# Kernel tuning notes

Measured on AMD Instinct MI355X. Metric: run time of the kernel, lower is better.

Reference implementation:

```python
import jax, jax.numpy as jnp
import numpy as np

B, T, C, H = 4, 2048, 1024, 16
HS = C // H  # head_size = 64


def setup_inputs() -> dict:
    key = jax.random.key(0)
    ks = jax.random.split(key, 6)
    s = C ** -0.5  # Linear default init scale (approx, kaiming-uniform-ish)
    x = jax.random.normal(ks[0], (B, T, C), dtype=jnp.float32)
    Wq = jax.random.normal(ks[1], (H, C, HS), dtype=jnp.float32) * s
    Wk = jax.random.normal(ks[2], (H, C, HS), dtype=jnp.float32) * s
    Wv = jax.random.normal(ks[3], (H, C, HS), dtype=jnp.float32) * s
    Wproj = jax.random.normal(ks[4], (C, C), dtype=jnp.float32) * s
    bproj = jax.random.normal(ks[5], (C,), dtype=jnp.float32) * s
    return {"x": x, "Wq": Wq, "Wk": Wk, "Wv": Wv, "Wproj": Wproj, "bproj": bproj}


def reference(x, Wq, Wk, Wv, Wproj, bproj):
    # Batched multi-head attention equivalent to looping over per-head modules.
    # q,k,v: (B, H, T, HS)
    q = jnp.einsum('btc,hcd->bhtd', x, Wq)
    k = jnp.einsum('btc,hcd->bhtd', x, Wk)
    v = jnp.einsum('btc,hcd->bhtd', x, Wv)
    scale = HS ** -0.5
    scores = jnp.einsum('bhqd,bhkd->bhqk', q, k) * scale  # (B,H,T,T)
    causal = jnp.tril(jnp.ones((T, T), dtype=bool))
    scores = jnp.where(causal, scores, -jnp.inf)
    wei = jax.nn.softmax(scores, axis=-1)
    out_heads = jnp.einsum('bhqk,bhkd->bhqd', wei, v)  # (B,H,T,HS)
    # concat heads along last dim -> (B,T,H*HS) = (B,T,C)
    combo = out_heads.transpose(0, 2, 1, 3).reshape(B, T, C)
    out = jnp.einsum('btc,cd->btd', combo, Wproj.T.T @ jnp.eye(C, dtype=combo.dtype)) if False else combo @ Wproj.T + bproj
    # dropout p=0.0 (eval) -> identity
    return out
```

## Files before the change

### kernel.cpp

```cpp
#include <hip/hip_runtime.h>
#include <stdint.h>

#define B_  4
#define T_  2048
#define C_  1024
#define H_  16
#define HS_ 64
#define M_  (B_*T_)
#define K_  C_

typedef unsigned short u16;
typedef float v4f __attribute__((ext_vector_type(4)));
typedef short v8s __attribute__((ext_vector_type(8)));
typedef u16   v4u __attribute__((ext_vector_type(4)));
typedef unsigned int u32;
typedef u32 v2u32 __attribute__((ext_vector_type(2)));

__device__ __forceinline__ u16 f2bf(float f){
  unsigned u = __float_as_uint(f);
  u += 0x7fffu + ((u >> 16) & 1u);
  return (u16)(u >> 16);
}

__device__ __forceinline__ u32 cvt_pk_bf16(float a, float b){
  u32 r;
  asm("v_cvt_pk_bf16_f32 %0, %1, %2" : "=v"(r) : "v"(a), "v"(b));
  return r;
}

__device__ __forceinline__ void async16(const void* g, void* l){
  __builtin_amdgcn_global_load_lds(
      (const __attribute__((address_space(1))) unsigned int*)g,
      (__attribute__((address_space(3))) unsigned int*)l,
      16, 0, 0);
}


__global__ void conv_blocked(const float* __restrict__ src, u16* __restrict__ dst){
  int gid = blockIdx.x * 256 + threadIdx.x;
  int r  = gid >> 7;
  int kg = gid & 127;
  const float* s = src + ((size_t)r << 10) + (kg << 3);
  v4f a = *(const v4f*)s;
  v4f b = *(const v4f*)(s + 4);
  union { v8s v; u16 e[8]; } o;
  o.e[0]=f2bf(a[0]); o.e[1]=f2bf(a[1]); o.e[2]=f2bf(a[2]); o.e[3]=f2bf(a[3]);
  o.e[4]=f2bf(b[0]); o.e[5]=f2bf(b[1]); o.e[6]=f2bf(b[2]); o.e[7]=f2bf(b[3]);
  *(v8s*)(dst + (((size_t)(r >> 4) * 128 + kg) * 128 + ((r & 15) << 3))) = o.v;
}

__global__ void transpose_w(const float* __restrict__ Wq, const float* __restrict__ Wk,
                            const float* __restrict__ Wv, u16* __restrict__ wallT){
  int idx = blockIdx.x * 256 + threadIdx.x;
  int n = idx >> 10, c = idx & 1023;
  int tensor = n >> 10;
  int h = (n >> 6) & 15;
  int d = n & 63;
  const float* W = (tensor == 0) ? Wq : ((tensor == 1) ? Wk : Wv);
  wallT[((size_t)(n >> 4) * 128 + (c >> 3)) * 128 + ((n & 15) << 3) + (c & 7)]
      = f2bf(W[((size_t)(h * C_ + c)) * HS_ + d]);
}

#define QSCALE 0.1803368801111204f

template<int MODE>
__global__ __launch_bounds__(256)
void gemm_bt(const u16* __restrict__ A, const u16* __restrict__ Bt,
             const float* __restrict__ bias,
             u16* __restrict__ o0, u16* __restrict__ o1, u16* __restrict__ o2,
             float* __restrict__ o0f)
{
  __shared__ __align__(16) u16 sA[2][128 * 32];
  __shared__ __align__(16) u16 sB[2][128 * 32];
  const int tid  = threadIdx.x;
  const int lane = tid & 63;
  const int wave = tid >> 6;
  const int l15  = lane & 15, quad = lane >> 4;
  const int wm   = wave >> 1, wn = wave & 1;
  const int m0   = blockIdx.y * 128;
  const int n0   = blockIdx.x * 128;
  const int mg0  = blockIdx.y * 8;
  const int ng0  = blockIdx.x * 8;

  v4f acc[4][4] = {};

  const int s0 = tid, s1 = tid + 256;
  const int t0 = s0 >> 6, r0 = s0 & 15, g0 = (s0 >> 4) & 3;
  const int t1 = s1 >> 6, r1 = s1 & 15, g1 = (s1 >> 4) & 3;

  const char* aS0 = (const char*)A  + ((size_t)(mg0 + t0) * 16384 + g0 * 128 + r0 * 8) * 2;
  const char* aS1 = (const char*)A  + ((size_t)(mg0 + t1) * 16384 + g1 * 128 + r1 * 8) * 2;
  const char* bS0 = (const char*)Bt + ((size_t)(ng0 + t0) * 16384 + g0 * 128 + r0 * 8) * 2;
  const char* bS1 = (const char*)Bt + ((size_t)(ng0 + t1) * 16384 + g1 * 128 + r1 * 8) * 2;

  async16(aS0, (char*)sA[0] + s0 * 16);
  async16(aS1, (char*)sA[0] + s1 * 16);
  async16(bS0, (char*)sB[0] + s0 * 16);
  async16(bS1, (char*)sB[0] + s1 * 16);
  __syncthreads();

  int cur = 0;
  for (int kk = 0; kk < K_; kk += 32){
    const int nxt = cur ^ 1;
    if (kk + 32 < K_){
      const size_t off = (size_t)(kk + 32) * 32;
      async16(aS0 + off, (char*)sA[nxt] + s0 * 16);
      async16(aS1 + off, (char*)sA[nxt] + s1 * 16);
      async16(bS0 + off, (char*)sB[nxt] + s0 * 16);
      async16(bS1 + off, (char*)sB[nxt] + s1 * 16);
    }

    v8s af[4], bfr[4];
    const u16* pa = sA[cur] + (size_t)(wm * 4) * 512 + lane * 8;
    const u16* pb = sB[cur] + (size_t)(wn * 4) * 512 + lane * 8;
    #pragma unroll
    for (int mi = 0; mi < 4; mi++) af[mi]  = *(const v8s*)(pa + mi * 512);
    #pragma unroll
    for (int ni = 0; ni < 4; ni++) bfr[ni] = *(const v8s*)(pb + ni * 512);

    #pragma unroll
    for (int mi = 0; mi < 4; mi++)
      #pragma unroll
      for (int ni = 0; ni < 4; ni++)
        acc[mi][ni] = __builtin_amdgcn_mfma_f32_16x16x32_bf16(af[mi], bfr[ni], acc[mi][ni], 0, 0, 0);

    __syncthreads();
    cur = nxt;
  }

  if constexpr (MODE == 0){
    #pragma unroll
    for (int ni = 0; ni < 4; ni++){
      const int ng = n0 + wn * 64 + ni * 16 + l15;
      const int tensor = ng >> 10;
      const int hh = (ng >> 6) & 15;
      const int d  = ng & 63;
      #pragma unroll
      for (int mi = 0; mi < 4; mi++){
        const int mbase = m0 + wm * 64 + mi * 16 + quad * 4;
        const int bb = mbase >> 11;
        const int tt = mbase & 2047;
        if (tensor == 2){
          v4u pk;
          #pragma unroll
          for (int r = 0; r < 4; r++) pk[r] = f2bf(acc[mi][ni][r]);
          *(v4u*)(o2 + ((size_t)((bb * H_ + hh) * HS_ + d)) * T_ + tt) = pk;
        } else if (tensor == 0){
          #pragma unroll
          for (int r = 0; r < 4; r++)
            o0[((size_t)((bb * H_ + hh)) * T_ + tt + r) * HS_ + d] = f2bf(acc[mi][ni][r] * QSCALE);
        } else {
          #pragma unroll
          for (int r = 0; r < 4; r++)
            o1[((size_t)((bb * H_ + hh)) * T_ + tt + r) * HS_ + d] = f2bf(acc[mi][ni][r]);
        }
      }
    }
  } else {
    #pragma unroll
    for (int ni = 0; ni < 4; ni++){
      const int ng = n0 + wn * 64 + ni * 16 + l15;
      const float bv = bias[ng];
      #pragma unroll
      for (int mi = 0; mi < 4; mi++){
        const int mbase = m0 + wm * 64 + mi * 16 + quad * 4;
        #pragma unroll
        for (int r = 0; r < 4; r++)
          o0f[(size_t)(mbase + r) * C_ + ng] = acc[mi][ni][r] + bv;
      }
    }
  }
}

__global__ __launch_bounds__(512, 4)
void attn(const u16* __restrict__ Q, const u16* __restrict__ Kb_, const u16* __restrict__ Vt,
          u16* __restrict__ O)
{
  __shared__ __align__(16) u16 sK[64 * 64];
  __shared__ __align__(16) u16 sV[64 * 64];
  __shared__ __align__(16) u16 Plds[8][16][88];
  const int tid  = threadIdx.x;
  const int lane = tid & 63;
  const int wave = tid >> 6;
  const int l15  = lane & 15, quad = lane >> 4;
  const int pp   = blockIdx.y & 7;
  const int bh   = blockIdx.x * 8 + (blockIdx.y >> 3);

  const u16* Qb = Q   + (size_t)bh * T_ * HS_;
  const u16* Kb = Kb_ + (size_t)bh * T_ * HS_;
  const u16* Vb = Vt  + (size_t)bh * HS_ * T_;
  const int b = bh >> 4, h = bh & 15;

  const int g  = tid;
  const int tg = g >> 3;
  const int sw = ((g & 7) ^ (tg & 7)) << 4;
  const char* Kby = (const char*)Kb;
  const char* Vby = (const char*)Vb;
  const int koff = tg * 128 + sw;
  const int voff = tg * (T_ * 2) + sw;
  char* sKp = (char*)sK + g * 16;
  char* sVp = (char*)sV + g * 16;

  const int fsw0 = (quad ^ (l15 & 7)) * 8;
  const int fsw1 = ((quad + 4) ^ (l15 & 7)) * 8;

  #pragma unroll 1
  for (int ph = 0; ph < 2; ph++){
    const int qt = ph ? (15 - pp) : pp;
    const int q0 = qt * 128 + wave * 16;

    const v8s qf0 = *(const v8s*)(Qb + (size_t)(q0 + l15) * HS_ + quad * 8);
    const v8s qf1 = *(const v8s*)(Qb + (size_t)(q0 + l15) * HS_ + 32 + quad * 8);

    v4f Oa[4] = {};
    float lsum = 0.f;

    const int ktmax = 2 * qt + 1;
    for (int kt = 0; kt <= ktmax; kt++){
      const int k0 = kt * 64;
      async16(Kby + (size_t)k0 * 128 + koff, sKp);
      async16(Vby + (size_t)k0 * 2   + voff, sVp);
      __syncthreads();

      if (k0 <= q0 + 15){
        v4f sacc[4] = {};
        __builtin_amdgcn_s_setprio(1);
        #pragma unroll
        for (int nt = 0; nt < 4; nt++){
          const u16* kr = sK + (nt * 16 + l15) * 64;
          v8s kf0 = *(const v8s*)(kr + fsw0);
          v8s kf1 = *(const v8s*)(kr + fsw1);
          sacc[nt] = __builtin_amdgcn_mfma_f32_16x16x32_bf16(kf0, qf0, sacc[nt], 0, 0, 0);
          sacc[nt] = __builtin_amdgcn_mfma_f32_16x16x32_bf16(kf1, qf1, sacc[nt], 0, 0, 0);
        }
        __builtin_amdgcn_s_setprio(0);
        const bool diag = (k0 + 63 > q0);
        const int qrow_rel = (q0 - k0) + l15;

        #pragma unroll
        for (int nt = 0; nt < 4; nt++){
          float p0 = exp2f(sacc[nt][0]);
          float p1 = exp2f(sacc[nt][1]);
          float p2 = exp2f(sacc[nt][2]);
          float p3 = exp2f(sacc[nt][3]);
          if (diag){
            const int kbase = nt * 16 + quad * 4;
            if (kbase + 0 > qrow_rel) p0 = 0.f;
            if (kbase + 1 > qrow_rel) p1 = 0.f;
            if (kbase + 2 > qrow_rel) p2 = 0.f;
            if (kbase + 3 > qrow_rel) p3 = 0.f;
          }
          lsum += (p0 + p1) + (p2 + p3);
          v2u32 w;
          w[0] = cvt_pk_bf16(p0, p1);
          w[1] = cvt_pk_bf16(p2, p3);
          *(v2u32*)&Plds[wave][l15][nt * 16 + quad * 4] = w;
        }

        asm volatile("" ::: "memory");
        const v8s pf0 = *(const v8s*)&Plds[wave][l15][quad * 8];
        const v8s pf1 = *(const v8s*)&Plds[wave][l15][32 + quad * 8];
        __builtin_amdgcn_s_setprio(1);
        #pragma unroll
        for (int nt = 0; nt < 4; nt++){
          const u16* vr = sV + (nt * 16 + l15) * 64;
          v8s vf0 = *(const v8s*)(vr + fsw0);
          v8s vf1 = *(const v8s*)(vr + fsw1);
          Oa[nt] = __builtin_amdgcn_mfma_f32_16x16x32_bf16(pf0, vf0, Oa[nt], 0, 0, 0);
          Oa[nt] = __builtin_amdgcn_mfma_f32_16x16x32_bf16(pf1, vf1, Oa[nt], 0, 0, 0);
        }
        __builtin_amdgcn_s_setprio(0);
      }
      __syncthreads();
    }

    float rs = lsum;
    rs += __shfl_xor(rs, 16);
    rs += __shfl_xor(rs, 32);
    const int mg = b * 128 + qt * 8 + wave;
    #pragma unroll
    for (int reg = 0; reg < 4; reg++){
      const float rsq = __shfl(rs, quad * 4 + reg);
      const float inv = (rsq > 0.f) ? (1.f / rsq) : 0.f;
      const int mrow = quad * 4 + reg;
      #pragma unroll
      for (int nt = 0; nt < 4; nt++){
        const int cg = h * 8 + nt * 2 + (l15 >> 3);
        O[((size_t)mg * 128 + cg) * 128 + mrow * 8 + (l15 & 7)] = f2bf(Oa[nt][reg] * inv);
      }
    }
  }
}

extern "C" void kernel_launch(void* const* d_in, const int* in_sizes, int n_in,
                              void* d_out, int out_size, void* d_ws, size_t ws_size,
                              hipStream_t stream)
{
  const float* x     = (const float*)d_in[0];
  const float* Wq    = (const float*)d_in[1];
  const float* Wk    = (const float*)d_in[2];
  const float* Wv    = (const float*)d_in[3];
  const float* Wproj = (const float*)d_in[4];
  const float* bproj = (const float*)d_in[5];
  float* out = (float*)d_out;

  u16* xhat   = (u16*)d_ws;
  u16* att    = xhat;
  u16* q_ws   = xhat  + (size_t)M_ * C_;
  u16* k_ws   = q_ws  + (size_t)M_ * C_;
  u16* vt_ws  = k_ws  + (size_t)M_ * C_;
  u16* wallT  = vt_ws + (size_t)M_ * C_;
  u16* wprojT = wallT + (size_t)3 * C_ * K_;

  conv_blocked<<<dim3((M_ * C_) / 8 / 256), dim3(256), 0, stream>>>(x, xhat);
  transpose_w<<<dim3((3 * C_ * K_) / 256), dim3(256), 0, stream>>>(Wq, Wk, Wv, wallT);
  conv_blocked<<<dim3((C_ * C_) / 8 / 256), dim3(256), 0, stream>>>(Wproj, wprojT);
  gemm_bt<0><<<dim3(24, 64), dim3(256), 0, stream>>>(xhat, wallT, nullptr,
                                                     q_ws, k_ws, vt_ws, nullptr);
  attn<<<dim3(8, 64), dim3(512), 0, stream>>>(q_ws, k_ws, vt_ws, att);
  gemm_bt<1><<<dim3(8, 64), dim3(256), 0, stream>>>(att, wprojT, bproj,
                                                    nullptr, nullptr, nullptr, out);
}
```

Measured before the change: 270.0 us.

## Triple-buffer GEMM loads and read V directly from global in attention

The projection GEMM moves from a double-buffered to a triple-buffered LDS pipeline. It prefetches two K-steps ahead and uses explicit vmcnt waits plus raw barriers in place of __syncthreads, aiming to hide global latency better. Separately, the attention kernel no longer stages V tiles through LDS; each wave loads its V fragments straight from global memory (L2/cache). This cuts LDS traffic and shared memory use, but adds redundant global reads across the 8 waves and exposes their latency inside the PV loop.

```diff
diff --git a/kernel.cpp b/kernel.cpp
--- a/kernel.cpp
+++ b/kernel.cpp
@@ -70,8 +70,8 @@
              u16* __restrict__ o0, u16* __restrict__ o1, u16* __restrict__ o2,
              float* __restrict__ o0f)
 {
-  __shared__ __align__(16) u16 sA[2][128 * 32];
-  __shared__ __align__(16) u16 sB[2][128 * 32];
+  __shared__ __align__(16) u16 sA[3][128 * 32];
+  __shared__ __align__(16) u16 sB[3][128 * 32];
   const int tid  = threadIdx.x;
   const int lane = tid & 63;
   const int wave = tid >> 6;
@@ -93,21 +93,27 @@
   const char* bS0 = (const char*)Bt + ((size_t)(ng0 + t0) * 16384 + g0 * 128 + r0 * 8) * 2;
   const char* bS1 = (const char*)Bt + ((size_t)(ng0 + t1) * 16384 + g1 * 128 + r1 * 8) * 2;
 
-  async16(aS0, (char*)sA[0] + s0 * 16);
-  async16(aS1, (char*)sA[0] + s1 * 16);
-  async16(bS0, (char*)sB[0] + s0 * 16);
-  async16(bS1, (char*)sB[0] + s1 * 16);
-  __syncthreads();
-
-  int cur = 0;
-  for (int kk = 0; kk < K_; kk += 32){
-    const int nxt = cur ^ 1;
-    if (kk + 32 < K_){
-      const size_t off = (size_t)(kk + 32) * 32;
-      async16(aS0 + off, (char*)sA[nxt] + s0 * 16);
-      async16(aS1 + off, (char*)sA[nxt] + s1 * 16);
-      async16(bS0 + off, (char*)sB[nxt] + s0 * 16);
-      async16(bS1 + off, (char*)sB[nxt] + s1 * 16);
+  async16(aS0,        (char*)sA[0] + s0 * 16);
+  async16(aS1,        (char*)sA[0] + s1 * 16);
+  async16(bS0,        (char*)sB[0] + s0 * 16);
+  async16(bS1,        (char*)sB[0] + s1 * 16);
+  async16(aS0 + 1024, (char*)sA[1] + s0 * 16);
+  async16(aS1 + 1024, (char*)sA[1] + s1 * 16);
+  async16(bS0 + 1024, (char*)sB[1] + s0 * 16);
+  async16(bS1 + 1024, (char*)sB[1] + s1 * 16);
+  asm volatile("s_waitcnt vmcnt(4)" ::: "memory");
+  __builtin_amdgcn_s_barrier();
+  asm volatile("" ::: "memory");
+  __builtin_amdgcn_sched_barrier(0);
+
+  int cur = 0, nx2 = 2;
+  for (int t = 0; t < K_ / 32; ++t){
+    if (t + 2 < K_ / 32){
+      const size_t off = (size_t)(t + 2) * 1024;
+      async16(aS0 + off, (char*)sA[nx2] + s0 * 16);
+      async16(aS1 + off, (char*)sA[nx2] + s1 * 16);
+      async16(bS0 + off, (char*)sB[nx2] + s0 * 16);
+      async16(bS1 + off, (char*)sB[nx2] + s1 * 16);
     }
 
     v8s af[4], bfr[4];
@@ -124,8 +130,13 @@
       for (int ni = 0; ni < 4; ni++)
         acc[mi][ni] = __builtin_amdgcn_mfma_f32_16x16x32_bf16(af[mi], bfr[ni], acc[mi][ni], 0, 0, 0);
 
-    __syncthreads();
-    cur = nxt;
+    if (t + 2 < K_ / 32) asm volatile("s_waitcnt vmcnt(4)" ::: "memory");
+    else                 asm volatile("s_waitcnt vmcnt(0)" ::: "memory");
+    __builtin_amdgcn_s_barrier();
+    asm volatile("" ::: "memory");
+    __builtin_amdgcn_sched_barrier(0);
+    cur = (cur == 2) ? 0 : cur + 1;
+    nx2 = (nx2 == 2) ? 0 : nx2 + 1;
   }
 
   if constexpr (MODE == 0){
@@ -177,7 +188,6 @@
           u16* __restrict__ O)
 {
   __shared__ __align__(16) u16 sK[64 * 64];
-  __shared__ __align__(16) u16 sV[64 * 64];
   __shared__ __align__(16) u16 Plds[8][16][88];
   const int tid  = threadIdx.x;
   const int lane = tid & 63;
@@ -195,11 +205,8 @@
   const int tg = g >> 3;
   const int sw = ((g & 7) ^ (tg & 7)) << 4;
   const char* Kby = (const char*)Kb;
-  const char* Vby = (const char*)Vb;
   const int koff = tg * 128 + sw;
-  const int voff = tg * (T_ * 2) + sw;
   char* sKp = (char*)sK + g * 16;
-  char* sVp = (char*)sV + g * 16;
 
   const int fsw0 = (quad ^ (l15 & 7)) * 8;
   const int fsw1 = ((quad + 4) ^ (l15 & 7)) * 8;
@@ -219,7 +226,6 @@
     for (int kt = 0; kt <= ktmax; kt++){
       const int k0 = kt * 64;
       async16(Kby + (size_t)k0 * 128 + koff, sKp);
-      async16(Vby + (size_t)k0 * 2   + voff, sVp);
       __syncthreads();
 
       if (k0 <= q0 + 15){
@@ -263,9 +269,9 @@
         __builtin_amdgcn_s_setprio(1);
         #pragma unroll
         for (int nt = 0; nt < 4; nt++){
-          const u16* vr = sV + (nt * 16 + l15) * 64;
-          v8s vf0 = *(const v8s*)(vr + fsw0);
-          v8s vf1 = *(const v8s*)(vr + fsw1);
+          const u16* vrow = Vb + (size_t)(nt * 16 + l15) * T_ + k0;
+          v8s vf0 = *(const v8s*)(vrow + quad * 8);
+          v8s vf1 = *(const v8s*)(vrow + 32 + quad * 8);
           Oa[nt] = __builtin_amdgcn_mfma_f32_16x16x32_bf16(pf0, vf0, Oa[nt], 0, 0, 0);
           Oa[nt] = __builtin_amdgcn_mfma_f32_16x16x32_bf16(pf1, vf1, Oa[nt], 0, 0, 0);
         }
```

Result: slower. 375.0 us (+38.9%).
